# Optimization experiments

Measured on AMD Instinct MI355X. Metric: run time of the kernel, lower is better.

## Reference

```python
import jax, jax.numpy as jnp
import numpy as np

B, S, D = 8, 4096, 512
L = 8921  # n_labels (ICD9 full)

def setup_inputs() -> dict:
    key = jax.random.key(0)
    kx, ku = jax.random.split(key)
    x = jax.random.normal(kx, (B, S, D), dtype=jnp.float32)
    # xavier_uniform init for U [L, D]
    bound = jnp.sqrt(6.0 / (L + D)).astype(jnp.float32)
    U = jax.random.uniform(ku, (L, D), dtype=jnp.float32, minval=-bound, maxval=bound)
    return {"x": x, "U": U}

def reference(x, U):
    # scores: [B, L, S] = U @ x^T (unscaled)
    scores = jnp.einsum('ld,bsd->bls', U, x)
    alpha = jax.nn.softmax(scores, axis=2)  # softmax over sequence dim
    out = jnp.einsum('bls,bsd->bld', alpha, x)  # [B, L, D]
    return (out, alpha)
```

## Files before the change

### kernel.cpp

```cpp
#include <hip/hip_runtime.h>
#include <stdint.h>
#include <stddef.h>

#define BB 8
#define SS 4096
#define DD 512
#define LL 8921

typedef __attribute__((ext_vector_type(8))) short bf16x8;
typedef __attribute__((ext_vector_type(4))) float f32x4;
typedef __attribute__((ext_vector_type(4))) unsigned short u16x4;
typedef __attribute__((ext_vector_type(8))) unsigned short u16x8;

__device__ __forceinline__ unsigned short f2bf(float f) {
  union { float f; uint32_t u; } v; v.f = f;
  uint32_t r = (v.u + 0x7FFFu + ((v.u >> 16) & 1u)) >> 16;
  return (unsigned short)r;
}

__device__ __forceinline__ float bf2f(unsigned short h) {
  union { uint32_t u; float f; } v; v.u = ((uint32_t)h) << 16;
  return v.f;
}

__device__ __forceinline__ void gload_lds16(const void* g, void* l) {
  __builtin_amdgcn_global_load_lds(
      (__attribute__((address_space(1))) void*)(void*)g,
      (__attribute__((address_space(3))) void*)l, 16, 0, 0);
}

__device__ __forceinline__ f32x4 mfma16(bf16x8 a, bf16x8 b, f32x4 c) {
  return __builtin_amdgcn_mfma_f32_16x16x32_bf16(a, b, c, 0, 0, 0);
}

__global__ __launch_bounds__(256) void k_cvtU(const float* __restrict__ U,
                                              unsigned short* __restrict__ Ub) {
  const int idx = blockIdx.x * 256 + threadIdx.x;
  const int nchunk = (LL * DD) / 8;
  if (idx >= nchunk) return;
  const float4* s = (const float4*)U + (size_t)idx * 2;
  const float4 a = s[0], b = s[1];
  u16x8 h;
  h[0] = f2bf(a.x); h[1] = f2bf(a.y); h[2] = f2bf(a.z); h[3] = f2bf(a.w);
  h[4] = f2bf(b.x); h[5] = f2bf(b.y); h[6] = f2bf(b.z); h[7] = f2bf(b.w);
  *(u16x8*)(Ub + (size_t)idx * 8) = h;
}

__global__ __launch_bounds__(256) void k_cvtx(const float* __restrict__ x,
                                              unsigned short* __restrict__ xb,
                                              unsigned short* __restrict__ xT) {
  __shared__ unsigned short t[64][72];
  const int b = blockIdx.z;
  const int s0 = blockIdx.x * 64;
  const int d0 = blockIdx.y * 64;
  const int tid = threadIdx.x;
  const int rr = tid >> 4;
  const int cv = tid & 15;
#pragma unroll
  for (int i = 0; i < 4; ++i) {
    const int srow = rr + i * 16;
    const size_t gi = ((size_t)b * SS + s0 + srow) * DD + d0 + cv * 4;
    const float4 v = *(const float4*)&x[gi];
    u16x4 h;
    h[0] = f2bf(v.x); h[1] = f2bf(v.y); h[2] = f2bf(v.z); h[3] = f2bf(v.w);
    *(u16x4*)&xb[gi] = h;
    t[srow][cv * 4 + 0] = h[0]; t[srow][cv * 4 + 1] = h[1];
    t[srow][cv * 4 + 2] = h[2]; t[srow][cv * 4 + 3] = h[3];
  }
  __syncthreads();
#pragma unroll
  for (int i = 0; i < 4; ++i) {
    const int drow = rr + i * 16;
    u16x4 h;
    h[0] = t[cv * 4 + 0][drow]; h[1] = t[cv * 4 + 1][drow];
    h[2] = t[cv * 4 + 2][drow]; h[3] = t[cv * 4 + 3][drow];
    *(u16x4*)&xT[((size_t)b * DD + d0 + drow) * SS + s0 + cv * 4] = h;
  }
}


__global__ __launch_bounds__(256) void k_score2(const unsigned short* __restrict__ Ub,
                                                const unsigned short* __restrict__ xb,
                                                unsigned short* __restrict__ es,
                                                float* __restrict__ Z) {
  __shared__ unsigned short smem[2][128][64];
  const int tid = threadIdx.x;
  const int lane = tid & 63, wid = tid >> 6;
  const int wr = wid >> 1, wc = wid & 1;
  const int b = blockIdx.y;
  const int lt = blockIdx.x >> 5, st = blockIdx.x & 31;
  const int l0 = lt * 128, s0 = st * 128;
  const int fr = lane & 15, fq = lane >> 4;
  const int swz = (fr & 7) * 8;

  f32x4 acc[4][4];
#pragma unroll
  for (int m = 0; m < 4; ++m)
#pragma unroll
    for (int n = 0; n < 4; ++n) acc[m][n] = (f32x4){0.f, 0.f, 0.f, 0.f};

  for (int k0 = 0; k0 < DD; k0 += 64) {
#pragma unroll
    for (int r = 0; r < 4; ++r) {
      const int c = r * 256 + tid;
      const int row = c >> 3;
      const int colsw = ((c & 7) ^ (row & 7)) * 8;
      int lrow = l0 + row; if (lrow > LL - 1) lrow = LL - 1;
      gload_lds16(Ub + (size_t)lrow * DD + k0 + colsw, (unsigned short*)smem[0] + c * 8);
      gload_lds16(xb + ((size_t)b * SS + s0 + row) * DD + k0 + colsw,
                  (unsigned short*)smem[1] + c * 8);
    }
    __syncthreads();
#pragma unroll
    for (int kk = 0; kk < 64; kk += 32) {
      bf16x8 af[4], bfv[4];
#pragma unroll
      for (int m = 0; m < 4; ++m)
        af[m] = *(const bf16x8*)((const unsigned short*)smem[0] +
                 (wr * 64 + m * 16 + fr) * 64 + ((kk + fq * 8) ^ swz));
#pragma unroll
      for (int n = 0; n < 4; ++n)
        bfv[n] = *(const bf16x8*)((const unsigned short*)smem[1] +
                 (wc * 64 + n * 16 + fr) * 64 + ((kk + fq * 8) ^ swz));
#pragma unroll
      for (int m = 0; m < 4; ++m)
#pragma unroll
        for (int n = 0; n < 4; ++n)
          acc[m][n] = mfma16(af[m], bfv[n], acc[m][n]);
    }
    __syncthreads();
  }

  float ev[4][4][4];
  float rsum[4][4];
#pragma unroll
  for (int m = 0; m < 4; ++m)
#pragma unroll
    for (int j = 0; j < 4; ++j) rsum[m][j] = 0.f;
#pragma unroll
  for (int m = 0; m < 4; ++m)
#pragma unroll
    for (int n = 0; n < 4; ++n)
#pragma unroll
      for (int j = 0; j < 4; ++j) {
        const float e = __expf(acc[m][n][j]);
        ev[m][n][j] = e;
        rsum[m][j] += e;
      }
#pragma unroll
  for (int m = 0; m < 4; ++m)
#pragma unroll
    for (int j = 0; j < 4; ++j) {
      float v = rsum[m][j];
      v += __shfl_xor(v, 1);
      v += __shfl_xor(v, 2);
      v += __shfl_xor(v, 4);
      v += __shfl_xor(v, 8);
      const int l = l0 + wr * 64 + m * 16 + fq * 4 + j;
      if (fr == 0 && l < LL) atomicAdd(&Z[b * LL + l], v);
    }
  unsigned short (*Es)[128] = (unsigned short (*)[128])smem;
#pragma unroll
  for (int m = 0; m < 4; ++m) {
    const int lr = wr * 64 + m * 16 + fq * 4;
#pragma unroll
    for (int n = 0; n < 4; ++n) {
      const int sc = wc * 64 + n * 16 + fr;
#pragma unroll
      for (int j = 0; j < 4; ++j) {
        const int ll = lr + j;
        Es[ll][sc ^ ((ll & 7) << 3)] = f2bf(ev[m][n][j]);
      }
    }
  }
  __syncthreads();
  {
    const int lr = tid >> 1;
    const int ch = (tid & 1) * 64;
    const int l = l0 + lr;
    if (l < LL) {
      unsigned short* dst = es + ((size_t)b * LL + l) * SS + s0 + ch;
#pragma unroll
      for (int w = 0; w < 8; ++w) {
        u16x8 hv = *(const u16x8*)&Es[lr][(ch + w * 8) ^ ((lr & 7) << 3)];
        *(u16x8*)(dst + w * 8) = hv;
      }
    }
  }
}

__global__ __launch_bounds__(256) void k_pv6(const unsigned short* __restrict__ es,
                                             const unsigned short* __restrict__ xTb,
                                             const float* __restrict__ Z,
                                             float* __restrict__ out,
                                             float* __restrict__ alpha) {
  __shared__ unsigned short As[2][128][64];
  __shared__ unsigned short Bs[2][128][64];
  const int tid = threadIdx.x;
  const int lane = tid & 63, wid = tid >> 6;
  const int wr = wid >> 1, wc = wid & 1;
  const int b = blockIdx.y;
  const int bid = blockIdx.x;
  const int logical = (bid & 7) * 35 + (bid >> 3);
  const int lt = logical >> 2, dt = logical & 3;
  const int l0 = lt * 128, d0 = dt * 128;
  const int fr = lane & 15, fq = lane >> 4;
  const int swz = (fr & 7) * 8;

  float rZrow[4];
#pragma unroll
  for (int r = 0; r < 4; ++r) {
    int lrow = l0 + ((r * 256 + tid) >> 3);
    if (lrow > LL - 1) lrow = LL - 1;
    rZrow[r] = 1.0f / Z[b * LL + lrow];
  }

  f32x4 acc[4][4];
#pragma unroll
  for (int m = 0; m < 4; ++m)
#pragma unroll
    for (int n = 0; n < 4; ++n) acc[m][n] = (f32x4){0.f, 0.f, 0.f, 0.f};

  auto STAGE = [&](unsigned short (*An)[64], unsigned short (*Bn)[64], int k0) {
#pragma unroll
    for (int r = 0; r < 4; ++r) {
      const int c = r * 256 + tid;
      const int row = c >> 3;
      const int colsw = ((c & 7) ^ (row & 7)) * 8;
      int lrow = l0 + row; if (lrow > LL - 1) lrow = LL - 1;
      gload_lds16(es + ((size_t)b * LL + lrow) * SS + k0 + colsw,
                  (unsigned short*)An + c * 8);
      gload_lds16(xTb + ((size_t)b * DD + d0 + row) * SS + k0 + colsw,
                  (unsigned short*)Bn + c * 8);
    }
  };

  auto BODY = [&](int t, unsigned short (*Ac)[64], unsigned short (*Bc)[64],
                  unsigned short (*An)[64], unsigned short (*Bn)[64]) {
    if (t < 63) STAGE(An, Bn, (t + 1) * 64);

    if ((t >> 4) == dt) {
      const int k0 = t * 64;
#pragma unroll
      for (int r = 0; r < 4; ++r) {
        const int c = r * 256 + tid;
        const int row = c >> 3;
        const int colg = ((c & 7) ^ (row & 7)) * 8;
        int lrow = l0 + row; if (lrow > LL - 1) lrow = LL - 1;
        const u16x8 h = *(const u16x8*)((unsigned short*)Ac + c * 8);
        const float rz = rZrow[r];
        float4 a, bv;
        a.x = bf2f(h[0]) * rz; a.y = bf2f(h[1]) * rz;
        a.z = bf2f(h[2]) * rz; a.w = bf2f(h[3]) * rz;
        bv.x = bf2f(h[4]) * rz; bv.y = bf2f(h[5]) * rz;
        bv.z = bf2f(h[6]) * rz; bv.w = bf2f(h[7]) * rz;
        float* dst = alpha + ((size_t)b * LL + lrow) * SS + k0 + colg;
        *(float4*)dst = a;
        *(float4*)(dst + 4) = bv;
      }
    }

    __builtin_amdgcn_s_setprio(1);
#pragma unroll
    for (int kk = 0; kk < 64; kk += 32) {
      bf16x8 af[4], bfv[4];
#pragma unroll
      for (int m = 0; m < 4; ++m)
        af[m] = *(const bf16x8*)((const unsigned short*)Ac +
                 (wr * 64 + m * 16 + fr) * 64 + ((kk + fq * 8) ^ swz));
#pragma unroll
      for (int n = 0; n < 4; ++n)
        bfv[n] = *(const bf16x8*)((const unsigned short*)Bc +
                 (wc * 64 + n * 16 + fr) * 64 + ((kk + fq * 8) ^ swz));
#pragma unroll
      for (int m = 0; m < 4; ++m)
#pragma unroll
        for (int n = 0; n < 4; ++n)
          acc[m][n] = mfma16(af[m], bfv[n], acc[m][n]);
    }
    __builtin_amdgcn_s_setprio(0);

    if (t < 63) {
      __builtin_amdgcn_sched_barrier(0);
      asm volatile("s_waitcnt vmcnt(0)" ::: "memory");
      __builtin_amdgcn_s_barrier();
      __builtin_amdgcn_sched_barrier(0);
    }
  };

  STAGE(As[0], Bs[0], 0);
  asm volatile("s_waitcnt vmcnt(0)" ::: "memory");
  __syncthreads();

  for (int tt = 0; tt < 32; ++tt) {
    BODY(2 * tt,     As[0], Bs[0], As[1], Bs[1]);
    BODY(2 * tt + 1, As[1], Bs[1], As[0], Bs[0]);
  }

  float rZv[4][4];
#pragma unroll
  for (int m = 0; m < 4; ++m)
#pragma unroll
    for (int j = 0; j < 4; ++j) {
      const int l = l0 + wr * 64 + m * 16 + fq * 4 + j;
      rZv[m][j] = (l < LL) ? (1.0f / Z[b * LL + l]) : 0.f;
    }
#pragma unroll
  for (int m = 0; m < 4; ++m) {
    const int lbase = l0 + wr * 64 + m * 16 + fq * 4;
#pragma unroll
    for (int n = 0; n < 4; ++n) {
      const int d = d0 + wc * 64 + n * 16 + fr;
#pragma unroll
      for (int j = 0; j < 4; ++j) {
        const int l = lbase + j;
        if (l < LL) out[((size_t)b * LL + l) * DD + d] = acc[m][n][j] * rZv[m][j];
      }
    }
  }
}


__global__ __launch_bounds__(256) void k_score(const unsigned short* __restrict__ Ub,
                                               const unsigned short* __restrict__ xb,
                                               float* __restrict__ alpha,
                                               float* __restrict__ Z) {
  __shared__ unsigned short As[128][64];
  __shared__ unsigned short Bs[128][64];
  const int tid = threadIdx.x;
  const int lane = tid & 63, wid = tid >> 6;
  const int wr = wid >> 1, wc = wid & 1;
  const int b = blockIdx.y;
  const int lt = blockIdx.x >> 5, st = blockIdx.x & 31;
  const int l0 = lt * 128, s0 = st * 128;
  const int fr = lane & 15, fq = lane >> 4;

  f32x4 acc[4][4];
#pragma unroll
  for (int m = 0; m < 4; ++m)
#pragma unroll
    for (int n = 0; n < 4; ++n) acc[m][n] = (f32x4){0.f, 0.f, 0.f, 0.f};

  for (int k0 = 0; k0 < DD; k0 += 64) {
#pragma unroll
    for (int r = 0; r < 4; ++r) {
      const int c = r * 256 + tid;
      const int row = c >> 3, col = (c & 7) * 8;
      int lrow = l0 + row; if (lrow > LL - 1) lrow = LL - 1;
      gload_lds16(Ub + (size_t)lrow * DD + k0 + col, (unsigned short*)As + c * 8);
      gload_lds16(xb + ((size_t)b * SS + s0 + row) * DD + k0 + col,
                  (unsigned short*)Bs + c * 8);
    }
    __syncthreads();
#pragma unroll
    for (int kk = 0; kk < 64; kk += 32) {
      bf16x8 af[4], bfv[4];
#pragma unroll
      for (int m = 0; m < 4; ++m)
        af[m] = *(const bf16x8*)&As[wr * 64 + m * 16 + fr][kk + fq * 8];
#pragma unroll
      for (int n = 0; n < 4; ++n)
        bfv[n] = *(const bf16x8*)&Bs[wc * 64 + n * 16 + fr][kk + fq * 8];
#pragma unroll
      for (int m = 0; m < 4; ++m)
#pragma unroll
        for (int n = 0; n < 4; ++n)
          acc[m][n] = mfma16(af[m], bfv[n], acc[m][n]);
    }
    __syncthreads();
  }

  float rsum[4][4];
#pragma unroll
  for (int m = 0; m < 4; ++m)
#pragma unroll
    for (int j = 0; j < 4; ++j) rsum[m][j] = 0.f;
#pragma unroll
  for (int m = 0; m < 4; ++m) {
    const int lbase = l0 + wr * 64 + m * 16 + fq * 4;
#pragma unroll
    for (int n = 0; n < 4; ++n) {
      const int s = s0 + wc * 64 + n * 16 + fr;
#pragma unroll
      for (int j = 0; j < 4; ++j) {
        const float e = __expf(acc[m][n][j]);
        rsum[m][j] += e;
        const int l = lbase + j;
        if (l < LL) alpha[((size_t)b * LL + l) * SS + s] = e;
      }
    }
  }
#pragma unroll
  for (int m = 0; m < 4; ++m)
#pragma unroll
    for (int j = 0; j < 4; ++j) {
      float v = rsum[m][j];
      v += __shfl_xor(v, 1);
      v += __shfl_xor(v, 2);
      v += __shfl_xor(v, 4);
      v += __shfl_xor(v, 8);
      const int l = l0 + wr * 64 + m * 16 + fq * 4 + j;
      if (fr == 0 && l < LL) atomicAdd(&Z[b * LL + l], v);
    }
}

__global__ __launch_bounds__(256) void k_scale(float* __restrict__ alpha,
                                               const float* __restrict__ Z) {
  const int row = blockIdx.x;
  const float rZ = 1.0f / Z[row];
  float4* p = (float4*)alpha + (size_t)row * (SS / 4);
  const int t = threadIdx.x;
#pragma unroll
  for (int i = 0; i < 4; ++i) {
    float4 v = p[t + i * 256];
    v.x *= rZ; v.y *= rZ; v.z *= rZ; v.w *= rZ;
    p[t + i * 256] = v;
  }
}

__global__ __launch_bounds__(256) void k_pv(const float* __restrict__ alpha,
                                            const unsigned short* __restrict__ xTb,
                                            float* __restrict__ out) {
  __shared__ unsigned short As[128][64];
  __shared__ unsigned short Bs[128][64];
  const int tid = threadIdx.x;
  const int lane = tid & 63, wid = tid >> 6;
  const int wr = wid >> 1, wc = wid & 1;
  const int b = blockIdx.y;
  const int lt = blockIdx.x >> 2, dt = blockIdx.x & 3;
  const int l0 = lt * 128, d0 = dt * 128;
  const int fr = lane & 15, fq = lane >> 4;

  f32x4 acc[4][4];
#pragma unroll
  for (int m = 0; m < 4; ++m)
#pragma unroll
    for (int n = 0; n < 4; ++n) acc[m][n] = (f32x4){0.f, 0.f, 0.f, 0.f};

  for (int k0 = 0; k0 < SS; k0 += 64) {
#pragma unroll
    for (int r = 0; r < 4; ++r) {
      const int c = r * 256 + tid;
      const int row = c >> 3, col = (c & 7) * 8;
      gload_lds16(xTb + ((size_t)b * DD + d0 + row) * SS + k0 + col,
                  (unsigned short*)Bs + c * 8);
      int lrow = l0 + row; if (lrow > LL - 1) lrow = LL - 1;
      const float* src = alpha + ((size_t)b * LL + lrow) * SS + k0 + col;
      const float4 v0 = *(const float4*)src;
      const float4 v1 = *(const float4*)(src + 4);
      bf16x8 h;
      h[0] = (short)f2bf(v0.x); h[1] = (short)f2bf(v0.y);
      h[2] = (short)f2bf(v0.z); h[3] = (short)f2bf(v0.w);
      h[4] = (short)f2bf(v1.x); h[5] = (short)f2bf(v1.y);
      h[6] = (short)f2bf(v1.z); h[7] = (short)f2bf(v1.w);
      *(bf16x8*)((unsigned short*)As + c * 8) = h;
    }
    __syncthreads();
#pragma unroll
    for (int kk = 0; kk < 64; kk += 32) {
      bf16x8 af[4], bfv[4];
#pragma unroll
      for (int m = 0; m < 4; ++m)
        af[m] = *(const bf16x8*)&As[wr * 64 + m * 16 + fr][kk + fq * 8];
#pragma unroll
      for (int n = 0; n < 4; ++n)
        bfv[n] = *(const bf16x8*)&Bs[wc * 64 + n * 16 + fr][kk + fq * 8];
#pragma unroll
      for (int m = 0; m < 4; ++m)
#pragma unroll
        for (int n = 0; n < 4; ++n)
          acc[m][n] = mfma16(af[m], bfv[n], acc[m][n]);
    }
    __syncthreads();
  }

#pragma unroll
  for (int m = 0; m < 4; ++m) {
    const int lbase = l0 + wr * 64 + m * 16 + fq * 4;
#pragma unroll
    for (int n = 0; n < 4; ++n) {
      const int d = d0 + wc * 64 + n * 16 + fr;
#pragma unroll
      for (int j = 0; j < 4; ++j) {
        const int l = lbase + j;
        if (l < LL) out[((size_t)b * LL + l) * DD + d] = acc[m][n][j];
      }
    }
  }
}

extern "C" void kernel_launch(void* const* d_in, const int* in_sizes, int n_in,
                              void* d_out, int out_size, void* d_ws, size_t ws_size,
                              hipStream_t stream) {
  const float* x = (const float*)d_in[0];
  const float* U = (const float*)d_in[1];
  float* out   = (float*)d_out;
  float* alpha = out + (size_t)BB * LL * DD;

  const size_t off_Z  = 0;
  const size_t off_U  = 285696;
  const size_t off_xb = 9420800;
  const size_t off_xT = 42975232;
  const size_t off_es = 76529664;
  const size_t es_bytes = (size_t)BB * LL * SS * 2;
  const size_t need_small = off_es;
  const size_t need_big   = off_es + es_bytes;

  if (ws_size < need_small) return;

  char* ws = (char*)d_ws;
  float* Z = (float*)(ws + off_Z);
  unsigned short* Ub = (unsigned short*)(ws + off_U);
  unsigned short* xb = (unsigned short*)(ws + off_xb);
  unsigned short* xT = (unsigned short*)(ws + off_xT);
  unsigned short* es = (unsigned short*)(ws + off_es);

  hipMemsetAsync(Z, 0, (size_t)BB * LL * 4, stream);
  k_cvtU<<<dim3(((LL * DD / 8) + 255) / 256), 256, 0, stream>>>(U, Ub);
  k_cvtx<<<dim3(SS / 64, DD / 64, BB), 256, 0, stream>>>(x, xb, xT);

  if (ws_size >= need_big) {
    k_score2<<<dim3(70 * 32, BB), 256, 0, stream>>>(Ub, xb, es, Z);
    k_pv6<<<dim3(70 * 4, BB), 256, 0, stream>>>(es, xT, Z, out, alpha);
  } else {
    k_score<<<dim3(70 * 32, BB), 256, 0, stream>>>(Ub, xb, alpha, Z);
    k_scale<<<dim3(BB * LL), 256, 0, stream>>>(alpha, Z);
    k_pv<<<dim3(70 * 4, BB), 256, 0, stream>>>(alpha, xT, out);
  }
}
```

Baseline: 1.366 ms.

## Deepen PV kernel pipeline to four-stage K=32 ring buffer

Replaces the double-buffered K=64 tiles in the P·V kernel with a four-slot ring of K=32 tiles, prefetching three steps ahead and waiting with partial vmcnt instead of draining all loads each iteration. Global offsets are precomputed per thread and the LDS swizzle is adjusted for the narrower rows. The aim is to hide global-load latency better, at the cost of twice as many barriers per K and smaller MFMA batches per sync.

```diff
diff --git a/kernel.cpp b/kernel.cpp
--- a/kernel.cpp
+++ b/kernel.cpp
@@ -189,13 +189,13 @@
   }
 }
 
-__global__ __launch_bounds__(256) void k_pv6(const unsigned short* __restrict__ es,
+__global__ __launch_bounds__(256) void k_pv7(const unsigned short* __restrict__ es,
                                              const unsigned short* __restrict__ xTb,
                                              const float* __restrict__ Z,
                                              float* __restrict__ out,
                                              float* __restrict__ alpha) {
-  __shared__ unsigned short As[2][128][64];
-  __shared__ unsigned short Bs[2][128][64];
+  __shared__ unsigned short A4[4][128][32];
+  __shared__ unsigned short B4[4][128][32];
   const int tid = threadIdx.x;
   const int lane = tid & 63, wid = tid >> 6;
   const int wr = wid >> 1, wc = wid & 1;
@@ -205,14 +205,22 @@
   const int lt = logical >> 2, dt = logical & 3;
   const int l0 = lt * 128, d0 = dt * 128;
   const int fr = lane & 15, fq = lane >> 4;
-  const int swz = (fr & 7) * 8;
-
-  float rZrow[4];
-#pragma unroll
-  for (int r = 0; r < 4; ++r) {
-    int lrow = l0 + ((r * 256 + tid) >> 3);
-    if (lrow > LL - 1) lrow = LL - 1;
-    rZrow[r] = 1.0f / Z[b * LL + lrow];
+  const int rdoff = (fq ^ ((fr >> 1) & 3)) * 8;
+
+  size_t esoff[2], xtoff[2], aloff[2];
+  int cdst[2];
+  float rZrow[2];
+#pragma unroll
+  for (int g = 0; g < 2; ++g) {
+    const int c = g * 256 + tid;
+    const int row = c >> 2;
+    const int jsw = ((c & 3) ^ ((row >> 1) & 3)) * 8;
+    int lrow = l0 + row; if (lrow > LL - 1) lrow = LL - 1;
+    esoff[g] = ((size_t)b * LL + lrow) * SS + jsw;
+    aloff[g] = esoff[g];
+    xtoff[g] = ((size_t)b * DD + d0 + row) * SS + jsw;
+    cdst[g] = c * 8;
+    rZrow[g] = 1.0f / Z[b * LL + lrow];
   }
 
   f32x4 acc[4][4];
@@ -221,80 +229,82 @@
 #pragma unroll
     for (int n = 0; n < 4; ++n) acc[m][n] = (f32x4){0.f, 0.f, 0.f, 0.f};
 
-  auto STAGE = [&](unsigned short (*An)[64], unsigned short (*Bn)[64], int k0) {
-#pragma unroll
-    for (int r = 0; r < 4; ++r) {
-      const int c = r * 256 + tid;
-      const int row = c >> 3;
-      const int colsw = ((c & 7) ^ (row & 7)) * 8;
-      int lrow = l0 + row; if (lrow > LL - 1) lrow = LL - 1;
-      gload_lds16(es + ((size_t)b * LL + lrow) * SS + k0 + colsw,
-                  (unsigned short*)An + c * 8);
-      gload_lds16(xTb + ((size_t)b * DD + d0 + row) * SS + k0 + colsw,
-                  (unsigned short*)Bn + c * 8);
+  auto STAGE = [&](int slot, int kt) {
+#pragma unroll
+    for (int g = 0; g < 2; ++g) {
+      gload_lds16(es + esoff[g] + kt * 32, (unsigned short*)A4[slot] + cdst[g]);
+      gload_lds16(xTb + xtoff[g] + kt * 32, (unsigned short*)B4[slot] + cdst[g]);
     }
   };
 
-  auto BODY = [&](int t, unsigned short (*Ac)[64], unsigned short (*Bc)[64],
-                  unsigned short (*An)[64], unsigned short (*Bn)[64]) {
-    if (t < 63) STAGE(An, Bn, (t + 1) * 64);
-
-    if ((t >> 4) == dt) {
-      const int k0 = t * 64;
-#pragma unroll
-      for (int r = 0; r < 4; ++r) {
-        const int c = r * 256 + tid;
-        const int row = c >> 3;
-        const int colg = ((c & 7) ^ (row & 7)) * 8;
-        int lrow = l0 + row; if (lrow > LL - 1) lrow = LL - 1;
-        const u16x8 h = *(const u16x8*)((unsigned short*)Ac + c * 8);
-        const float rz = rZrow[r];
-        float4 a, bv;
-        a.x = bf2f(h[0]) * rz; a.y = bf2f(h[1]) * rz;
-        a.z = bf2f(h[2]) * rz; a.w = bf2f(h[3]) * rz;
-        bv.x = bf2f(h[4]) * rz; bv.y = bf2f(h[5]) * rz;
-        bv.z = bf2f(h[6]) * rz; bv.w = bf2f(h[7]) * rz;
-        float* dst = alpha + ((size_t)b * LL + lrow) * SS + k0 + colg;
-        *(float4*)dst = a;
-        *(float4*)(dst + 4) = bv;
-      }
-    }
-
+  auto ALPHA = [&](int slot, int t) {
+#pragma unroll
+    for (int g = 0; g < 2; ++g) {
+      const u16x8 h = *(const u16x8*)((const unsigned short*)A4[slot] + cdst[g]);
+      const float rz = rZrow[g];
+      float4 a, bv;
+      a.x = bf2f(h[0]) * rz; a.y = bf2f(h[1]) * rz;
+      a.z = bf2f(h[2]) * rz; a.w = bf2f(h[3]) * rz;
+      bv.x = bf2f(h[4]) * rz; bv.y = bf2f(h[5]) * rz;
+      bv.z = bf2f(h[6]) * rz; bv.w = bf2f(h[7]) * rz;
+      float* dst = alpha + aloff[g] + t * 32;
+      *(float4*)dst = a;
+      *(float4*)(dst + 4) = bv;
+    }
+  };
+
+  auto COMPUTE = [&](int slot) {
+    const unsigned short* Ab = (const unsigned short*)A4[slot];
+    const unsigned short* Bb = (const unsigned short*)B4[slot];
+    bf16x8 af[4], bfv[4];
+#pragma unroll
+    for (int m = 0; m < 4; ++m)
+      af[m] = *(const bf16x8*)(Ab + (wr * 64 + m * 16 + fr) * 32 + rdoff);
+#pragma unroll
+    for (int n = 0; n < 4; ++n)
+      bfv[n] = *(const bf16x8*)(Bb + (wc * 64 + n * 16 + fr) * 32 + rdoff);
     __builtin_amdgcn_s_setprio(1);
 #pragma unroll
-    for (int kk = 0; kk < 64; kk += 32) {
-      bf16x8 af[4], bfv[4];
-#pragma unroll
-      for (int m = 0; m < 4; ++m)
-        af[m] = *(const bf16x8*)((const unsigned short*)Ac +
-                 (wr * 64 + m * 16 + fr) * 64 + ((kk + fq * 8) ^ swz));
+    for (int m = 0; m < 4; ++m)
 #pragma unroll
       for (int n = 0; n < 4; ++n)
-        bfv[n] = *(const bf16x8*)((const unsigned short*)Bc +
-                 (wc * 64 + n * 16 + fr) * 64 + ((kk + fq * 8) ^ swz));
-#pragma unroll
-      for (int m = 0; m < 4; ++m)
-#pragma unroll
-        for (int n = 0; n < 4; ++n)
-          acc[m][n] = mfma16(af[m], bfv[n], acc[m][n]);
-    }
+        acc[m][n] = mfma16(af[m], bfv[n], acc[m][n]);
     __builtin_amdgcn_s_setprio(0);
-
-    if (t < 63) {
-      __builtin_amdgcn_sched_barrier(0);
-      asm volatile("s_waitcnt vmcnt(0)" ::: "memory");
-      __builtin_amdgcn_s_barrier();
-      __builtin_amdgcn_sched_barrier(0);
-    }
   };
 
-  STAGE(As[0], Bs[0], 0);
-  asm volatile("s_waitcnt vmcnt(0)" ::: "memory");
+  STAGE(0, 0); STAGE(1, 1); STAGE(2, 2);
+  asm volatile("s_waitcnt vmcnt(8)" ::: "memory");
   __syncthreads();
 
-  for (int tt = 0; tt < 32; ++tt) {
-    BODY(2 * tt,     As[0], Bs[0], As[1], Bs[1]);
-    BODY(2 * tt + 1, As[1], Bs[1], As[0], Bs[0]);
+  for (int t = 0; t < 125; ++t) {
+    const int s = t & 3;
+    STAGE((t + 3) & 3, t + 3);
+    if ((t >> 5) == dt) ALPHA(s, t);
+    COMPUTE(s);
+    __builtin_amdgcn_sched_barrier(0);
+    asm volatile("s_waitcnt vmcnt(8)" ::: "memory");
+    __builtin_amdgcn_s_barrier();
+    __builtin_amdgcn_sched_barrier(0);
+  }
+  {
+    if ((125 >> 5) == dt) ALPHA(125 & 3, 125);
+    COMPUTE(125 & 3);
+    __builtin_amdgcn_sched_barrier(0);
+    asm volatile("s_waitcnt vmcnt(4)" ::: "memory");
+    __builtin_amdgcn_s_barrier();
+    __builtin_amdgcn_sched_barrier(0);
+  }
+  {
+    if ((126 >> 5) == dt) ALPHA(126 & 3, 126);
+    COMPUTE(126 & 3);
+    __builtin_amdgcn_sched_barrier(0);
+    asm volatile("s_waitcnt vmcnt(0)" ::: "memory");
+    __builtin_amdgcn_s_barrier();
+    __builtin_amdgcn_sched_barrier(0);
+  }
+  {
+    if ((127 >> 5) == dt) ALPHA(127 & 3, 127);
+    COMPUTE(127 & 3);
   }
 
   float rZv[4][4];
@@ -521,7 +531,7 @@
 
   if (ws_size >= need_big) {
     k_score2<<<dim3(70 * 32, BB), 256, 0, stream>>>(Ub, xb, es, Z);
-    k_pv6<<<dim3(70 * 4, BB), 256, 0, stream>>>(es, xT, Z, out, alpha);
+    k_pv7<<<dim3(70 * 4, BB), 256, 0, stream>>>(es, xT, Z, out, alpha);
   } else {
     k_score<<<dim3(70 * 32, BB), 256, 0, stream>>>(Ub, xb, alpha, Z);
     k_scale<<<dim3(BB * LL), 256, 0, stream>>>(alpha, Z);
```

After: 1.444 ms. 5.7% more time.
